# Performance work log

Measured on AMD Instinct MI355X. Metric: run time of the kernel, lower is better.

Reference implementation:

```python
import jax, jax.numpy as jnp
import numpy as np

N, D = 8192, 768
EPS = 1e-5  # torch LayerNorm default


def setup_inputs() -> dict:
    key = jax.random.key(0)
    ks = jax.random.split(key, 5)
    q = jax.random.normal(ks[0], (N, D), dtype=jnp.float32)
    k = jax.random.normal(ks[1], (N, D), dtype=jnp.float32)
    v = jax.random.normal(ks[2], (N, D), dtype=jnp.float32)
    ln_w = jnp.ones((D,), dtype=jnp.float32)
    ln_b = jnp.zeros((D,), dtype=jnp.float32)
    W_qkv = jax.random.normal(ks[3], (D, D), dtype=jnp.float32) * 0.02
    W_proj = jax.random.normal(ks[4], (D, D), dtype=jnp.float32) * 0.02
    b_proj = jnp.zeros((D,), dtype=jnp.float32)
    return {"q": q, "k": k, "v": v, "ln_w": ln_w, "ln_b": ln_b,
            "W_qkv": W_qkv, "W_proj": W_proj, "b_proj": b_proj}


def reference(q, k, v, ln_w, ln_b, W_qkv, W_proj, b_proj):
    dim = q.shape[-1]
    scale = dim ** (-0.5)

    def ln(x):
        mu = jnp.mean(x, axis=-1, keepdims=True)
        var = jnp.mean((x - mu) ** 2, axis=-1, keepdims=True)
        return (x - mu) * jax.lax.rsqrt(var + EPS) * ln_w + ln_b

    # shared LayerNorm + shared Linear (toto0, no bias) applied to q, k, v
    qn = ln(q) @ W_qkv.T  # [N, D]
    kn = ln(k) @ W_qkv.T
    vn = ln(v) @ W_qkv.T

    attn = jnp.einsum('qc,kc->qk', qn, kn) * scale  # [N, N]
    attn = jax.nn.softmax(attn, axis=-1)
    out = jnp.einsum('qk,kc->qc', attn, vn)  # [N, D]
    out = out @ W_proj.T + b_proj  # proj0
    return out
```

## Files before the change

kernel.cpp:

```cpp
#include <hip/hip_runtime.h>
#include <hip/hip_bf16.h>
#include <stdint.h>

typedef short bf16x8 __attribute__((ext_vector_type(8)));
typedef float f32x4 __attribute__((ext_vector_type(4)));
typedef unsigned short u16;
typedef u16 u16x8 __attribute__((ext_vector_type(8)));

__device__ __forceinline__ u16 f2bf(float x) {
  __hip_bfloat16 h = __float2bfloat16(x);
  return *reinterpret_cast<u16*>(&h);
}
__device__ __forceinline__ float bf2f(u16 v) {
  unsigned u = (unsigned)v << 16;
  return *reinterpret_cast<float*>(&u);
}

__device__ __forceinline__ void gload_lds16(const void* g, const void* lds_base) {
  __builtin_amdgcn_global_load_lds(
      (const __attribute__((address_space(1))) unsigned int*)(uintptr_t)g,
      (__attribute__((address_space(3))) unsigned int*)(uintptr_t)lds_base,
      16, 0, 0);
}

#define BAR() __builtin_amdgcn_s_barrier()

__global__ __launch_bounds__(256) void ln_cast_kernel(
    const float* __restrict__ q, const float* __restrict__ k, const float* __restrict__ v,
    const float* __restrict__ lw, const float* __restrict__ lb, u16* __restrict__ out) {
  int row = blockIdx.x;
  const float* x;
  if (row < 8192) x = q + (size_t)row * 768;
  else if (row < 16384) x = k + (size_t)(row - 8192) * 768;
  else x = v + (size_t)(row - 16384) * 768;
  int t = threadIdx.x;
  __shared__ float red[4];
  __shared__ float red2[4];
  float4 a = (t < 192) ? ((const float4*)x)[t] : make_float4(0.f, 0.f, 0.f, 0.f);
  float s = a.x + a.y + a.z + a.w;
  for (int o = 32; o; o >>= 1) s += __shfl_down(s, o, 64);
  if ((t & 63) == 0) red[t >> 6] = s;
  __syncthreads();
  float mean = (red[0] + red[1] + red[2]) * (1.0f / 768.0f);
  float4 d = make_float4(a.x - mean, a.y - mean, a.z - mean, a.w - mean);
  float vs = (t < 192) ? (d.x * d.x + d.y * d.y + d.z * d.z + d.w * d.w) : 0.f;
  for (int o = 32; o; o >>= 1) vs += __shfl_down(vs, o, 64);
  if ((t & 63) == 0) red2[t >> 6] = vs;
  __syncthreads();
  float var = (red2[0] + red2[1] + red2[2]) * (1.0f / 768.0f);
  float rstd = rsqrtf(var + 1e-5f);
  if (t < 192) {
    float4 wv = ((const float4*)lw)[t];
    float4 bv = ((const float4*)lb)[t];
    ushort4 o;
    o.x = f2bf(d.x * rstd * wv.x + bv.x);
    o.y = f2bf(d.y * rstd * wv.y + bv.y);
    o.z = f2bf(d.z * rstd * wv.z + bv.z);
    o.w = f2bf(d.w * rstd * wv.w + bv.w);
    ((ushort4*)(out + (size_t)row * 768))[t] = o;
  }
}

__global__ __launch_bounds__(256) void cast_f32_bf16(const float* __restrict__ in,
                                                     u16* __restrict__ out, int n4) {
  int i = blockIdx.x * 256 + threadIdx.x;
  if (i < n4) {
    float4 vv = ((const float4*)in)[i];
    ushort4 o;
    o.x = f2bf(vv.x); o.y = f2bf(vv.y); o.z = f2bf(vv.z); o.w = f2bf(vv.w);
    ((ushort4*)out)[i] = o;
  }
}

__global__ __launch_bounds__(256) void zero_f32(float* __restrict__ p, int n) {
  int i = blockIdx.x * 256 + threadIdx.x;
  if (i < n) p[i] = 0.0f;
}

__global__ __launch_bounds__(256) void transpose64(const u16* __restrict__ in, u16* __restrict__ out) {
  __shared__ __align__(16) u16 tile[64][72];
  int b = blockIdx.x;
  int tr = b / 12, tc = b % 12;
  int t = threadIdx.x;
  int r = t >> 3;
  int cb = (t & 7) << 3;
#pragma unroll
  for (int i = 0; i < 2; i++) {
    int row = r + i * 32;
    const u16* src = in + (size_t)(tr * 64 + row) * 768 + tc * 64 + cb;
    *(uint4*)&tile[row][cb] = *(const uint4*)src;
  }
  __syncthreads();
#pragma unroll
  for (int i = 0; i < 2; i++) {
    int oc = r + i * 32;
    u16x8 tmp;
#pragma unroll
    for (int j = 0; j < 8; j++) tmp[j] = tile[cb + j][oc];
    u16* dst = out + (size_t)(tc * 64 + oc) * 8192 + tr * 64 + cb;
    *(u16x8*)dst = tmp;
  }
}

__global__ __launch_bounds__(256) void reduce4_scale(
    const u16* __restrict__ p0, const u16* __restrict__ p1,
    const u16* __restrict__ p2, const u16* __restrict__ p3,
    const float* __restrict__ rowsum, u16* __restrict__ out, int n8) {
  int i = blockIdx.x * 256 + threadIdx.x;
  if (i < n8) {
    float inv = 1.0f / rowsum[i / 96];
    u16x8 a = ((const u16x8*)p0)[i];
    u16x8 b = ((const u16x8*)p1)[i];
    u16x8 c = ((const u16x8*)p2)[i];
    u16x8 d = ((const u16x8*)p3)[i];
    u16x8 o;
#pragma unroll
    for (int j = 0; j < 8; j++)
      o[j] = f2bf((bf2f(a[j]) + bf2f(b[j]) + bf2f(c[j]) + bf2f(d[j])) * inv);
    ((u16x8*)out)[i] = o;
  }
}

__global__ __launch_bounds__(512, 2) void qk_exp_256(
    const u16* __restrict__ A, const u16* __restrict__ B, u16* __restrict__ C,
    float* __restrict__ rowsum, float scale) {
  __shared__ __align__(16) u16 lds[8 * 256 * 32];
  int orig = blockIdx.x;
  int xcd = orig & 7, i = orig >> 3;
  int tm = xcd * 4 + (i & 3), tn = i >> 2;
  const int t = threadIdx.x, l = t & 63, w = t >> 6;
  const int wr = w >> 2, wc = w & 3;
  const int lr = l & 15, lq = l >> 4;
  const int colb = lq * 16;

  f32x4 acc[8][4];
#pragma unroll
  for (int m = 0; m < 8; m++)
#pragma unroll
    for (int n = 0; n < 4; n++) acc[m][n] = (f32x4){0.f, 0.f, 0.f, 0.f};

  const size_t rA0 = (size_t)tm * 256, rB0 = (size_t)tn * 256;

  const char* gsrc[4];
  int ldsoff[4];
#pragma unroll
  for (int idx = 0; idx < 4; idx++) {
    const u16* src = (idx < 2) ? A : B;
    size_t r0 = (idx < 2) ? rA0 : rB0;
    int p = idx & 1;
    int x = p * 8192 + t * 16;
    int r = x >> 6;
    int cb = (x & 63) ^ (((r >> 1) & 3) << 4);
    gsrc[idx] = (const char*)(src + (r0 + r) * 768) + cb;
    ldsoff[idx] = ((idx < 2) ? 0 : 65536) + p * 8192 + w * 1024;
  }
  int offA[2][4], offB[4];
#pragma unroll
  for (int mh = 0; mh < 2; mh++)
#pragma unroll
    for (int mf = 0; mf < 4; mf++) {
      int row = wr * 128 + (mh * 4 + mf) * 16 + lr;
      int x = row * 64 + colb;
      offA[mh][mf] = x ^ (((row >> 1) & 3) << 4);
    }
#pragma unroll
  for (int nf = 0; nf < 4; nf++) {
    int row = wc * 64 + nf * 16 + lr;
    int x = row * 64 + colb;
    offB[nf] = 65536 + (x ^ (((row >> 1) & 3) << 4));
  }

#define SCALL(BUF, TT, IDX)                                                  \
  gload_lds16(gsrc[IDX] + (size_t)(TT) * 64,                                 \
              (const char*)lds + (BUF) * 16384 + ldsoff[IDX])

  auto LOADA = [&](bf16x8 (&aF)[4], int b, int mh) {
#pragma unroll
    for (int mf = 0; mf < 4; mf++)
      aF[mf] = *(const bf16x8*)((const char*)lds + b * 16384 + offA[mh][mf]);
  };
  auto LOADB = [&](bf16x8 (&bF)[4], int b) {
#pragma unroll
    for (int nf = 0; nf < 4; nf++)
      bF[nf] = *(const bf16x8*)((const char*)lds + b * 16384 + offB[nf]);
  };
  auto MM32 = [&](bf16x8 (&aF)[4], bf16x8 (&aG)[4], bf16x8 (&bF)[4]) {
    __builtin_amdgcn_s_setprio(1);
#pragma unroll
    for (int mf = 0; mf < 4; mf++)
#pragma unroll
      for (int nf = 0; nf < 4; nf++)
        acc[mf][nf] = __builtin_amdgcn_mfma_f32_16x16x32_bf16(
            aF[mf], bF[nf], acc[mf][nf], 0, 0, 0);
#pragma unroll
    for (int mf = 0; mf < 4; mf++)
#pragma unroll
      for (int nf = 0; nf < 4; nf++)
        acc[4 + mf][nf] = __builtin_amdgcn_mfma_f32_16x16x32_bf16(
            aG[mf], bF[nf], acc[4 + mf][nf], 0, 0, 0);
    __builtin_amdgcn_s_setprio(0);
  };

#define PHASE(CUR, SBUF, STAGET, DOSTAGE, VMN)                               \
  do {                                                                       \
    bf16x8 aF[4], aG[4], bF[4];                                              \
    LOADA(aF, CUR, 0);                                                       \
    LOADA(aG, CUR, 1);                                                       \
    LOADB(bF, CUR);                                                          \
    if (DOSTAGE) {                                                           \
      SCALL(SBUF, STAGET, 0); SCALL(SBUF, STAGET, 1);                        \
      SCALL(SBUF, STAGET, 2); SCALL(SBUF, STAGET, 3);                        \
    }                                                                        \
    BAR();                                                                   \
    MM32(aF, aG, bF);                                                        \
    if ((VMN) == 8) asm volatile("s_waitcnt vmcnt(8)" ::: "memory");         \
    else if ((VMN) == 4) asm volatile("s_waitcnt vmcnt(4)" ::: "memory");    \
    else if ((VMN) == 0) asm volatile("s_waitcnt vmcnt(0)" ::: "memory");    \
    BAR();                                                                   \
  } while (0)

  SCALL(0, 0, 0); SCALL(0, 0, 1); SCALL(0, 0, 2); SCALL(0, 0, 3);
  SCALL(1, 1, 0); SCALL(1, 1, 1); SCALL(1, 1, 2); SCALL(1, 1, 3);
  SCALL(2, 2, 0); SCALL(2, 2, 1); SCALL(2, 2, 2); SCALL(2, 2, 3);
  asm volatile("s_waitcnt vmcnt(8)" ::: "memory");
  BAR();

  for (int Tb = 0; Tb < 20; Tb += 4) {
    PHASE(0, 3, Tb + 3, 1, 8);
    PHASE(1, 0, Tb + 4, 1, 8);
    PHASE(2, 1, Tb + 5, 1, 8);
    PHASE(3, 2, Tb + 6, 1, 8);
  }
  PHASE(0, 3, 23, 1, 8);
  PHASE(1, 0, 0, 0, 4);
  PHASE(2, 0, 0, 0, 0);
  PHASE(3, 0, 0, 0, -1);

#undef PHASE
#undef SCALL

  float rs[8][4];
#pragma unroll
  for (int m = 0; m < 8; m++)
#pragma unroll
    for (int j = 0; j < 4; j++) rs[m][j] = 0.0f;
  const size_t rowBase = rA0 + (size_t)wr * 128;
  const int colBase = tn * 256 + wc * 64;
#pragma unroll
  for (int mi = 0; mi < 8; mi++) {
    size_t row0 = rowBase + mi * 16 + lq * 4;
#pragma unroll
    for (int nf = 0; nf < 4; nf++) {
      int col = colBase + nf * 16 + lr;
#pragma unroll
      for (int j = 0; j < 4; j++) {
        float e = __expf(acc[mi][nf][j] * scale);
        C[(row0 + j) * 8192 + col] = f2bf(e);
        rs[mi][j] += e;
      }
    }
  }
#pragma unroll
  for (int mi = 0; mi < 8; mi++)
#pragma unroll
    for (int j = 0; j < 4; j++) {
      float r = rs[mi][j];
      r += __shfl_xor(r, 1); r += __shfl_xor(r, 2);
      r += __shfl_xor(r, 4); r += __shfl_xor(r, 8);
      if (lr == 0) atomicAdd(&rowsum[rowBase + mi * 16 + lq * 4 + j], r);
    }
}

template <int MODE>
__global__ __launch_bounds__(256, 2) void gemm_bt(
    const u16* __restrict__ A0, const u16* __restrict__ B0,
    void* __restrict__ Cv0, void* __restrict__ Cv1,
    int M, int N, int K, int lda, int ldb, int ldc,
    float scale, const float* __restrict__ bias, size_t cSplitStride) {
  __shared__ __align__(16) u16 sA[128 * 64];
  __shared__ __align__(16) u16 sB[128 * 64];
  const int z = blockIdx.y;
  const u16* A = A0 + (size_t)z * (size_t)K;
  const u16* B = B0 + (size_t)z * (size_t)K;
  u16* Cb = (z < 2) ? ((u16*)Cv0 + (size_t)z * cSplitStride)
                    : ((u16*)Cv1 + (size_t)(z - 2) * cSplitStride);
  const int nTn = N >> 7;
  int nwg = gridDim.x, orig = blockIdx.x;
  int qq = nwg >> 3, rr = nwg & 7;
  int xcd = orig & 7, loc = orig >> 3;
  int wg = (xcd < rr ? xcd * (qq + 1) : rr * (qq + 1) + (xcd - rr) * qq) + loc;
  int tm = wg / nTn, tn = wg % nTn;

  const int t = threadIdx.x, l = t & 63, w = t >> 6;
  const int wr = w >> 1, wc = w & 1;
  const int lr = l & 15, kg = (l >> 4) << 3;

  f32x4 acc[4][4];
#pragma unroll
  for (int m = 0; m < 4; m++)
#pragma unroll
    for (int n = 0; n < 4; n++) acc[m][n] = (f32x4){0.f, 0.f, 0.f, 0.f};

  const size_t rowA0 = (size_t)tm * 128;
  const size_t rowB0 = (size_t)tn * 128;
  const int nk = K >> 6;
  for (int kt = 0; kt < nk; kt++) {
    const int k0 = kt << 6;
#pragma unroll
    for (int i = 0; i < 4; i++) {
      int chunk = i * 256 + t;
      int row = chunk >> 3;
      int col = (chunk & 7) << 3;
      gload_lds16(A + (rowA0 + row) * lda + k0 + col, (const char*)sA + (i * 256 + w * 64) * 16);
      gload_lds16(B + (rowB0 + row) * ldb + k0 + col, (const char*)sB + (i * 256 + w * 64) * 16);
    }
    __syncthreads();
#pragma unroll
    for (int kk = 0; kk < 2; kk++) {
      bf16x8 af[4], bfv[4];
#pragma unroll
      for (int m = 0; m < 4; m++)
        af[m] = *(const bf16x8*)&sA[(wr * 64 + m * 16 + lr) * 64 + kk * 32 + kg];
#pragma unroll
      for (int n = 0; n < 4; n++)
        bfv[n] = *(const bf16x8*)&sB[(wc * 64 + n * 16 + lr) * 64 + kk * 32 + kg];
#pragma unroll
      for (int m = 0; m < 4; m++)
#pragma unroll
        for (int n = 0; n < 4; n++)
          acc[m][n] = __builtin_amdgcn_mfma_f32_16x16x32_bf16(af[m], bfv[n], acc[m][n], 0, 0, 0);
    }
    __syncthreads();
  }
#pragma unroll
  for (int m = 0; m < 4; m++) {
    int row = tm * 128 + wr * 64 + m * 16 + ((l >> 4) << 2);
#pragma unroll
    for (int n = 0; n < 4; n++) {
      int col = tn * 128 + wc * 64 + n * 16 + lr;
#pragma unroll
      for (int j = 0; j < 4; j++) {
        float vl = acc[m][n][j];
        if (MODE == 0) Cb[(size_t)(row + j) * ldc + col] = f2bf(vl * scale);
        else ((float*)Cv0)[(size_t)(row + j) * ldc + col] = vl + bias[col];
      }
    }
  }
}

extern "C" void kernel_launch(void* const* d_in, const int* in_sizes, int n_in,
                              void* d_out, int out_size, void* d_ws, size_t ws_size,
                              hipStream_t stream) {
  const float* q  = (const float*)d_in[0];
  const float* k  = (const float*)d_in[1];
  const float* v  = (const float*)d_in[2];
  const float* lw = (const float*)d_in[3];
  const float* lb = (const float*)d_in[4];
  const float* Wq = (const float*)d_in[5];
  const float* Wp = (const float*)d_in[6];
  const float* bp = (const float*)d_in[7];

  char* ws = (char*)d_ws;
  size_t off = 0;
  auto alloc = [&](size_t b) { size_t o = off; off += (b + 255) & ~(size_t)255; return o; };
  size_t o_ln = alloc((size_t)24576 * 768 * 2);
  size_t o_pj = alloc((size_t)24576 * 768 * 2);
  size_t o_wq = alloc((size_t)768 * 768 * 2);
  size_t o_wp = alloc((size_t)768 * 768 * 2);
  u16* lnbuf = (u16*)(ws + o_ln);
  u16* pj    = (u16*)(ws + o_pj);
  u16* wqb   = (u16*)(ws + o_wq);
  u16* wpb   = (u16*)(ws + o_wp);
  const size_t NS = (size_t)8192 * 768;
  u16* vnT = lnbuf;
  u16* p0  = lnbuf + NS;
  u16* p1  = lnbuf + 2 * NS;
  float* rowsum = (float*)(pj + 2 * NS);
  u16* p2 = (u16*)d_out;
  u16* p3 = p2 + NS;
  size_t fixedEnd = off;
  u16* Sbuf = (u16*)(ws + fixedEnd);

  const float scale = 0.03608439182435161f;

  ln_cast_kernel<<<dim3(24576), dim3(256), 0, stream>>>(q, k, v, lw, lb, lnbuf);
  cast_f32_bf16<<<dim3(576), dim3(256), 0, stream>>>(Wq, wqb, 147456);
  cast_f32_bf16<<<dim3(576), dim3(256), 0, stream>>>(Wp, wpb, 147456);

  gemm_bt<0><<<dim3(1152), dim3(256), 0, stream>>>(lnbuf, wqb, (void*)pj, (void*)pj,
      24576, 768, 768, 768, 768, 768, 1.0f, (const float*)nullptr, 0);

  transpose64<<<dim3(1536), dim3(256), 0, stream>>>(pj + (size_t)16384 * 768, vnT);
  zero_f32<<<dim3(32), dim3(256), 0, stream>>>(rowsum, 8192);

  qk_exp_256<<<dim3(1024), dim3(512), 0, stream>>>(pj, pj + NS, Sbuf, rowsum, scale);

  gemm_bt<0><<<dim3(384, 4), dim3(256), 0, stream>>>(
      Sbuf, vnT, (void*)p0, (void*)p2,
      8192, 768, 2048, 8192, 8192, 768, 1.0f, (const float*)nullptr, NS);

  reduce4_scale<<<dim3(3072), dim3(256), 0, stream>>>(p0, p1, p2, p3, rowsum, p0, (int)(NS / 8));

  gemm_bt<2><<<dim3(384), dim3(256), 0, stream>>>(p0, wpb, d_out, d_out,
      8192, 768, 768, 768, 768, 768, 1.0f, bp, 0);
}
```

Baseline: 358.8 us.

## Switch QK-exp kernel to double-buffered LDS and raise occupancy hint

Replaces the 4-stage LDS pipeline in the QK^T+exp kernel with a 2-stage double buffer, shrinking LDS from 128KB to 64KB per block. The launch bounds hint moves from 2 to 4 blocks per CU to use the freed LDS for more resident waves. In exchange, each K-step now waits on its prefetch with vmcnt(0), which leaves less memory latency hidden per block. Register pressure may also rise under the tighter launch bound.

```diff
diff --git a/kernel.cpp b/kernel.cpp
--- a/kernel.cpp
+++ b/kernel.cpp
@@ -121,10 +121,10 @@
   }
 }
 
-__global__ __launch_bounds__(512, 2) void qk_exp_256(
+__global__ __launch_bounds__(512, 4) void qk_exp_256(
     const u16* __restrict__ A, const u16* __restrict__ B, u16* __restrict__ C,
     float* __restrict__ rowsum, float scale) {
-  __shared__ __align__(16) u16 lds[8 * 256 * 32];
+  __shared__ __align__(16) u16 lds[2 * 2 * 8192];
   int orig = blockIdx.x;
   int xcd = orig & 7, i = orig >> 3;
   int tm = xcd * 4 + (i & 3), tn = i >> 2;
@@ -152,7 +152,7 @@
     int r = x >> 6;
     int cb = (x & 63) ^ (((r >> 1) & 3) << 4);
     gsrc[idx] = (const char*)(src + (r0 + r) * 768) + cb;
-    ldsoff[idx] = ((idx < 2) ? 0 : 65536) + p * 8192 + w * 1024;
+    ldsoff[idx] = ((idx < 2) ? 0 : 16384) + p * 8192 + w * 1024;
   }
   int offA[2][4], offB[4];
 #pragma unroll
@@ -167,22 +167,22 @@
   for (int nf = 0; nf < 4; nf++) {
     int row = wc * 64 + nf * 16 + lr;
     int x = row * 64 + colb;
-    offB[nf] = 65536 + (x ^ (((row >> 1) & 3) << 4));
+    offB[nf] = 16384 + (x ^ (((row >> 1) & 3) << 4));
   }
 
 #define SCALL(BUF, TT, IDX)                                                  \
   gload_lds16(gsrc[IDX] + (size_t)(TT) * 64,                                 \
-              (const char*)lds + (BUF) * 16384 + ldsoff[IDX])
+              (const char*)lds + (BUF) * 32768 + ldsoff[IDX])
 
   auto LOADA = [&](bf16x8 (&aF)[4], int b, int mh) {
 #pragma unroll
     for (int mf = 0; mf < 4; mf++)
-      aF[mf] = *(const bf16x8*)((const char*)lds + b * 16384 + offA[mh][mf]);
+      aF[mf] = *(const bf16x8*)((const char*)lds + b * 32768 + offA[mh][mf]);
   };
   auto LOADB = [&](bf16x8 (&bF)[4], int b) {
 #pragma unroll
     for (int nf = 0; nf < 4; nf++)
-      bF[nf] = *(const bf16x8*)((const char*)lds + b * 16384 + offB[nf]);
+      bF[nf] = *(const bf16x8*)((const char*)lds + b * 32768 + offB[nf]);
   };
   auto MM32 = [&](bf16x8 (&aF)[4], bf16x8 (&aG)[4], bf16x8 (&bF)[4]) {
     __builtin_amdgcn_s_setprio(1);
@@ -201,42 +201,26 @@
     __builtin_amdgcn_s_setprio(0);
   };
 
-#define PHASE(CUR, SBUF, STAGET, DOSTAGE, VMN)                               \
-  do {                                                                       \
-    bf16x8 aF[4], aG[4], bF[4];                                              \
-    LOADA(aF, CUR, 0);                                                       \
-    LOADA(aG, CUR, 1);                                                       \
-    LOADB(bF, CUR);                                                          \
-    if (DOSTAGE) {                                                           \
-      SCALL(SBUF, STAGET, 0); SCALL(SBUF, STAGET, 1);                        \
-      SCALL(SBUF, STAGET, 2); SCALL(SBUF, STAGET, 3);                        \
-    }                                                                        \
-    BAR();                                                                   \
-    MM32(aF, aG, bF);                                                        \
-    if ((VMN) == 8) asm volatile("s_waitcnt vmcnt(8)" ::: "memory");         \
-    else if ((VMN) == 4) asm volatile("s_waitcnt vmcnt(4)" ::: "memory");    \
-    else if ((VMN) == 0) asm volatile("s_waitcnt vmcnt(0)" ::: "memory");    \
-    BAR();                                                                   \
-  } while (0)
-
   SCALL(0, 0, 0); SCALL(0, 0, 1); SCALL(0, 0, 2); SCALL(0, 0, 3);
-  SCALL(1, 1, 0); SCALL(1, 1, 1); SCALL(1, 1, 2); SCALL(1, 1, 3);
-  SCALL(2, 2, 0); SCALL(2, 2, 1); SCALL(2, 2, 2); SCALL(2, 2, 3);
-  asm volatile("s_waitcnt vmcnt(8)" ::: "memory");
+  asm volatile("s_waitcnt vmcnt(0)" ::: "memory");
   BAR();
 
-  for (int Tb = 0; Tb < 20; Tb += 4) {
-    PHASE(0, 3, Tb + 3, 1, 8);
-    PHASE(1, 0, Tb + 4, 1, 8);
-    PHASE(2, 1, Tb + 5, 1, 8);
-    PHASE(3, 2, Tb + 6, 1, 8);
-  }
-  PHASE(0, 3, 23, 1, 8);
-  PHASE(1, 0, 0, 0, 4);
-  PHASE(2, 0, 0, 0, 0);
-  PHASE(3, 0, 0, 0, -1);
-
-#undef PHASE
+  for (int T = 0; T < 24; T++) {
+    const int cur = T & 1, nxt = cur ^ 1;
+    bf16x8 aF[4], aG[4], bF[4];
+    LOADA(aF, cur, 0);
+    LOADA(aG, cur, 1);
+    LOADB(bF, cur);
+    if (T < 23) {
+      SCALL(nxt, T + 1, 0); SCALL(nxt, T + 1, 1);
+      SCALL(nxt, T + 1, 2); SCALL(nxt, T + 1, 3);
+    }
+    BAR();
+    MM32(aF, aG, bF);
+    asm volatile("s_waitcnt vmcnt(0)" ::: "memory");
+    BAR();
+  }
+
 #undef SCALL
 
   float rs[8][4];
```

New measurement: 1.340 ms. 274% more time.
